# Kernel optimization log

Hardware: AMD Instinct MI355X
Metric: run time of the kernel (lower is better)

The kernel has to match this reference:

```python
import jax, jax.numpy as jnp
import numpy as np

N_NODES = 100000
N_EDGES = 1600000


def setup_inputs() -> dict:
    key = jax.random.key(0)
    k1, k2, k3, k4 = jax.random.split(key, 4)
    x = jax.random.normal(k1, (N_NODES, 16), dtype=jnp.float32)
    edge_index = jax.random.randint(k2, (2, N_EDGES), 0, N_NODES, dtype=jnp.int32)
    # Glorot-ish init for the two GCN layers
    W1 = jax.random.normal(k3, (16, 32), dtype=jnp.float32) * (1.0 / np.sqrt(16))
    b1 = jnp.zeros((32,), dtype=jnp.float32)
    W2 = jax.random.normal(k4, (32, 2), dtype=jnp.float32) * (1.0 / np.sqrt(32))
    b2 = jnp.zeros((2,), dtype=jnp.float32)
    return {"x": x, "edge_index": edge_index, "W1": W1, "b1": b1, "W2": W2, "b2": b2}


def _gcn_conv(x, W, b, src, dst, norm, n_nodes):
    # PyG GCNConv: h = X @ W; aggregate norm * h[src] at dst; add bias.
    h = x @ W                                   # [N, out]
    msg = h[src] * norm[:, None]                # [E+N, out] gather + scale
    out = jax.ops.segment_sum(msg, dst, num_segments=n_nodes)
    return out + b


def reference(x, edge_index, W1, b1, W2, b2):
    n = x.shape[0]
    self_loops = jnp.arange(n, dtype=edge_index.dtype)
    src = jnp.concatenate([edge_index[0], self_loops])  # [E+N]
    dst = jnp.concatenate([edge_index[1], self_loops])
    # Symmetric GCN normalization: deg computed on graph with self-loops
    deg = jax.ops.segment_sum(jnp.ones_like(dst, dtype=x.dtype), dst, num_segments=n)
    dis = jnp.where(deg > 0, jax.lax.rsqrt(deg), 0.0)   # deg^{-1/2}
    norm = dis[src] * dis[dst]                          # [E+N]

    h = jax.nn.relu(_gcn_conv(x, W1, b1, src, dst, norm, n))
    out = _gcn_conv(h, W2, b2, src, dst, norm, n)
    return out
```

## Files before the change

kernel.cpp:

```cpp
#include <hip/hip_runtime.h>
#include <hip/hip_fp16.h>

static constexpr int N  = 100000;
static constexpr int E  = 1600000;
static constexpr int B  = 256;
static constexpr int BG = 512;

static constexpr int BC     = 1024;
static constexpr int NBLKC  = 256;
static constexpr int CHUNKC = E / NBLKC;
static constexpr int CH2    = CHUNKC / 2;
static constexpr int PER2   = (CH2 + BC - 1) / BC;
static constexpr int NBUCK  = (N + 127) / 128;
static constexpr int SLAB   = 3072;
static constexpr int GCS    = 16;


__global__ __launch_bounds__(BC) void kC_scatter(
        const int2* __restrict__ src2, const int2* __restrict__ dst2,
        int* __restrict__ gcur, int* __restrict__ gslab) {
    __shared__ int lhist[NBUCK];
    __shared__ int gb[NBUCK];

    int t = threadIdx.x, blk = blockIdx.x;
    for (int i = t; i < NBUCK; i += BC) lhist[i] = 0;
    __syncthreads();

    int eb2 = blk * CH2;
    int2 dsv[PER2], ssv[PER2];
#pragma unroll
    for (int k = 0; k < PER2; ++k) {
        int idx = k * BC + t;
        if (idx < CH2) {
            dsv[k] = dst2[eb2 + idx];
            ssv[k] = src2[eb2 + idx];
            atomicAdd(&lhist[dsv[k].x >> 7], 1);
            atomicAdd(&lhist[dsv[k].y >> 7], 1);
        }
    }
    __syncthreads();

    if (t < NBUCK) {
        int h = lhist[t];
        if (h > 0) gb[t] = t * SLAB + atomicAdd(&gcur[t * GCS], h);
        lhist[t] = 0;
    }
    __syncthreads();

#pragma unroll
    for (int k = 0; k < PER2; ++k) {
        int idx = k * BC + t;
        if (idx < CH2) {
            {
                int d = dsv[k].x, b = d >> 7;
                int r = atomicAdd(&lhist[b], 1);
                int g = gb[b] + r;
                if (g < (b + 1) * SLAB)
                    gslab[g] = ssv[k].x | ((d & 127) << 17);
            }
            {
                int d = dsv[k].y, b = d >> 7;
                int r = atomicAdd(&lhist[b], 1);
                int g = gb[b] + r;
                if (g < (b + 1) * SLAB)
                    gslab[g] = ssv[k].y | ((d & 127) << 17);
            }
        }
    }
}


__global__ void kD1_deg(const int* __restrict__ gcur, const int* __restrict__ gslab,
                        int* __restrict__ rofs, const float4* __restrict__ x4,
                        __half* __restrict__ xpre) {
    __shared__ int c[128];
    __shared__ int wq[2];
    int t = threadIdx.x, b = blockIdx.x;
    if (t < 128) c[t] = 0;
    __syncthreads();

    int ne = min(gcur[b * GCS], SLAB);
    int base = b * SLAB;
    int ne4 = ne & ~3;
    for (int k = 4 * t; k < ne4; k += 4 * B) {
        int4 p4 = *(const int4*)(gslab + base + k);
        atomicAdd(&c[p4.x >> 17], 1);
        atomicAdd(&c[p4.y >> 17], 1);
        atomicAdd(&c[p4.z >> 17], 1);
        atomicAdd(&c[p4.w >> 17], 1);
    }
    if (t < ne - ne4) atomicAdd(&c[gslab[base + ne4 + t] >> 17], 1);
    __syncthreads();

    int lane = t & 63, wv = t >> 6;
    int val = (t < 128) ? c[t] : 0;
    int inc = val;
#pragma unroll
    for (int off = 1; off < 64; off <<= 1) {
        int u = __shfl_up(inc, off, 64);
        if (lane >= off) inc += u;
    }
    if (t == 63) wq[0] = inc;
    __syncthreads();
    if (t < 128) rofs[b * 129 + t] = base + inc - val + ((wv == 1) ? wq[0] : 0);
    if (t == 128) rofs[b * 129 + 128] = base + ne;

    int n = b * 128 + (t >> 1), h = t & 1;
    if (n < N) {
        float d = rsqrtf((float)(c[t >> 1] + 1));
        float4 u0 = x4[(size_t)n * 4 + h * 2];
        float4 u1 = x4[(size_t)n * 4 + h * 2 + 1];
        ushort4 p0, p1;
        p0.x = __half_as_ushort(__float2half(u0.x * d));
        p0.y = __half_as_ushort(__float2half(u0.y * d));
        p0.z = __half_as_ushort(__float2half(u0.z * d));
        p0.w = __half_as_ushort(__float2half(u0.w * d));
        p1.x = __half_as_ushort(__float2half(u1.x * d));
        p1.y = __half_as_ushort(__float2half(u1.y * d));
        p1.z = __half_as_ushort(__float2half(u1.z * d));
        p1.w = __half_as_ushort(__float2half(u1.w * d));
        *(ushort4*)(xpre + (size_t)n * 16 + h * 8)     = p0;
        *(ushort4*)(xpre + (size_t)n * 16 + h * 8 + 4) = p1;
    }
}


__global__ __launch_bounds__(BG) void kD2_agg(
        const __half* __restrict__ xpre, int* __restrict__ gslab,
        const int* __restrict__ rofs, const float* __restrict__ W1,
        const float* __restrict__ b1, const float* __restrict__ W2,
        float2* __restrict__ hpre) {
    __shared__ int st1[SLAB];
    __shared__ int cur[128];
    __shared__ int lofs[129];
    __shared__ float acc[128 * 17];
    __shared__ float sW1[512], sb1[32], sW2[64];
    int t = threadIdx.x, b = blockIdx.x;
    sW1[t] = W1[t];
    if (t < 32) sb1[t] = b1[t];
    if (t < 64) sW2[t] = W2[t];
    if (t < 128) cur[t] = 0;
    int base = b * SLAB;
    if (t < 129) lofs[t] = rofs[b * 129 + t] - base;
    __syncthreads();

    int ne = lofs[128];
    for (int k = t; k < ne; k += BG) {
        int p = gslab[base + k];
        int lo = p >> 17;
        int r = atomicAdd(&cur[lo], 1);
        st1[lofs[lo] + r] = p & 0x1FFFF;
    }
    __syncthreads();

    int ne4 = ne & ~3;
    for (int k = 4 * t; k < ne4; k += 4 * BG)
        *(int4*)(gslab + base + k) = *(const int4*)(st1 + k);
    for (int k = ne4 + t; k < ne; k += BG)
        gslab[base + k] = st1[k];

    int h = t & 1, e = (t >> 1) & 1, nl = t >> 2;
    int n = b * 128 + nl;
    float a0 = 0.f, a1 = 0.f, a2 = 0.f, a3 = 0.f,
          a4 = 0.f, a5 = 0.f, a6 = 0.f, a7 = 0.f;
    if (n < N) {
        auto add8 = [&](int4 w) {
            float2 q0 = __half22float2(*(__half2*)&w.x);
            float2 q1 = __half22float2(*(__half2*)&w.y);
            float2 q2 = __half22float2(*(__half2*)&w.z);
            float2 q3 = __half22float2(*(__half2*)&w.w);
            a0 += q0.x; a1 += q0.y; a2 += q1.x; a3 += q1.y;
            a4 += q2.x; a5 += q2.y; a6 += q3.x; a7 += q3.y;
        };
        int rs = lofs[nl], re = lofs[nl + 1];
        if (e == 0)
            add8(*(const int4*)(xpre + (size_t)n * 16 + h * 8));
        int k = rs + e;
        for (; k + 6 < re; k += 8) {
            int s0 = st1[k], s1 = st1[k + 2], s2 = st1[k + 4], s3 = st1[k + 6];
            int4 v0 = *(const int4*)(xpre + (size_t)s0 * 16 + h * 8);
            int4 v1 = *(const int4*)(xpre + (size_t)s1 * 16 + h * 8);
            int4 v2 = *(const int4*)(xpre + (size_t)s2 * 16 + h * 8);
            int4 v3 = *(const int4*)(xpre + (size_t)s3 * 16 + h * 8);
            add8(v0); add8(v1); add8(v2); add8(v3);
        }
        for (; k < re; k += 2)
            add8(*(const int4*)(xpre + (size_t)st1[k] * 16 + h * 8));
    }
    a0 += __shfl_xor(a0, 2, 64); a1 += __shfl_xor(a1, 2, 64);
    a2 += __shfl_xor(a2, 2, 64); a3 += __shfl_xor(a3, 2, 64);
    a4 += __shfl_xor(a4, 2, 64); a5 += __shfl_xor(a5, 2, 64);
    a6 += __shfl_xor(a6, 2, 64); a7 += __shfl_xor(a7, 2, 64);
    if (n < N && e == 0) {
        float* row = acc + nl * 17 + h * 8;
        row[0] = a0; row[1] = a1; row[2] = a2; row[3] = a3;
        row[4] = a4; row[5] = a5; row[6] = a6; row[7] = a7;
    }
    __syncthreads();

    if (t < 128) {
        int n2 = b * 128 + t;
        if (n2 < N) {
            int deg = lofs[t + 1] - lofs[t];
            float d = rsqrtf((float)(deg + 1));
            const float* row = acc + t * 17;
            float xi[16];
#pragma unroll
            for (int k = 0; k < 16; ++k) xi[k] = row[k] * d;
            float o0 = 0.f, o1 = 0.f;
#pragma unroll
            for (int c = 0; c < 32; ++c) {
                float hh = sb1[c];
#pragma unroll
                for (int k = 0; k < 16; ++k) hh = fmaf(xi[k], sW1[k * 32 + c], hh);
                hh = fmaxf(hh, 0.f);
                o0 = fmaf(hh, sW2[c * 2 + 0], o0);
                o1 = fmaf(hh, sW2[c * 2 + 1], o1);
            }
            hpre[n2] = make_float2(d * o0, d * o1);
        }
    }
}


__global__ __launch_bounds__(BG) void kF_l2(
        const float2* __restrict__ hpre, const int* __restrict__ gslab,
        const int* __restrict__ rofs, const float* __restrict__ b2,
        float2* __restrict__ out) {
    __shared__ int st1[SLAB];
    __shared__ int lofs[129];
    int t = threadIdx.x, b = blockIdx.x;
    int base = b * SLAB;
    if (t < 129) lofs[t] = rofs[b * 129 + t] - base;
    __syncthreads();

    int ne = lofs[128];
    int ne4 = ne & ~3;
    for (int k = 4 * t; k < ne4; k += 4 * BG)
        *(int4*)(st1 + k) = *(const int4*)(gslab + base + k);
    for (int k = ne4 + t; k < ne; k += BG)
        st1[k] = gslab[base + k];
    __syncthreads();

    int e = t & 3, nl = t >> 2;
    int n = b * 128 + nl;
    float o0 = 0.f, o1 = 0.f;
    int deg = 0;
    if (n < N) {
        int rs = lofs[nl], re = lofs[nl + 1];
        deg = re - rs;
        if (e == 0) {
            float2 self = hpre[n];
            o0 = self.x; o1 = self.y;
        }
        int k = rs + e;
        for (; k + 12 < re; k += 16) {
            float2 v0 = hpre[st1[k]];
            float2 v1 = hpre[st1[k + 4]];
            float2 v2 = hpre[st1[k + 8]];
            float2 v3 = hpre[st1[k + 12]];
            o0 += (v0.x + v1.x) + (v2.x + v3.x);
            o1 += (v0.y + v1.y) + (v2.y + v3.y);
        }
        for (; k < re; k += 4) {
            float2 v = hpre[st1[k]];
            o0 += v.x; o1 += v.y;
        }
    }
    o0 += __shfl_xor(o0, 1, 64); o1 += __shfl_xor(o1, 1, 64);
    o0 += __shfl_xor(o0, 2, 64); o1 += __shfl_xor(o1, 2, 64);
    if (n < N && e == 0) {
        float d = rsqrtf((float)(deg + 1));
        out[n] = make_float2(fmaf(d, o0, b2[0]), fmaf(d, o1, b2[1]));
    }
}


extern "C" void kernel_launch(void* const* d_in, const int* in_sizes, int n_in,
                              void* d_out, int out_size, void* d_ws, size_t ws_size,
                              hipStream_t stream) {
    const float* x  = (const float*)d_in[0];
    const int*   ei = (const int*)d_in[1];
    const float* W1 = (const float*)d_in[2];
    const float* b1 = (const float*)d_in[3];
    const float* W2 = (const float*)d_in[4];
    const float* b2 = (const float*)d_in[5];

    const int2* src2 = (const int2*)ei;
    const int2* dst2 = (const int2*)(ei + E);

    int*    gslab = (int*)d_ws;
    int*    rofs  = gslab + (size_t)NBUCK * SLAB;
    int*    gcur  = rofs + 100880;
    float*  hpre  = (float*)(gcur + 12512);
    __half* xpre  = (__half*)(hpre + 2 * (size_t)N);

    hipMemsetAsync(gcur, 0, NBUCK * GCS * sizeof(int), stream);
    kC_scatter<<<NBLKC, BC, 0, stream>>>(src2, dst2, gcur, gslab);
    kD1_deg<<<NBUCK, B, 0, stream>>>(gcur, gslab, rofs, (const float4*)x, xpre);
    kD2_agg<<<NBUCK, BG, 0, stream>>>(xpre, gslab, rofs, W1, b1, W2, (float2*)hpre);
    kF_l2<<<NBUCK, BG, 0, stream>>>((const float2*)hpre, gslab, rofs, b2,
                                    (float2*)d_out);
}
```

Baseline: 129.0 us.

## Count node degrees via global atomics in scatter, simplify degree kernel to scan

Moves per-node degree counting into the scatter kernel using global atomics on a new deg array, so the second kernel no longer re-reads the slab to build histograms. The second kernel becomes a per-node scan with one thread per node, writing row offsets and prescaled half-precision features. The scatter grid is also enlarged to 500 blocks. This trades a slab re-read for about 1.6M scattered global atomics, which may contend.

```diff
diff --git a/kernel.cpp b/kernel.cpp
--- a/kernel.cpp
+++ b/kernel.cpp
@@ -3,11 +3,11 @@
 
 static constexpr int N  = 100000;
 static constexpr int E  = 1600000;
-static constexpr int B  = 256;
+static constexpr int B1 = 128;
 static constexpr int BG = 512;
 
 static constexpr int BC     = 1024;
-static constexpr int NBLKC  = 256;
+static constexpr int NBLKC  = 500;
 static constexpr int CHUNKC = E / NBLKC;
 static constexpr int CH2    = CHUNKC / 2;
 static constexpr int PER2   = (CH2 + BC - 1) / BC;
@@ -18,7 +18,8 @@
 
 __global__ __launch_bounds__(BC) void kC_scatter(
         const int2* __restrict__ src2, const int2* __restrict__ dst2,
-        int* __restrict__ gcur, int* __restrict__ gslab) {
+        int* __restrict__ gcur, int* __restrict__ gslab,
+        int* __restrict__ deg) {
     __shared__ int lhist[NBUCK];
     __shared__ int gb[NBUCK];
 
@@ -36,6 +37,8 @@
             ssv[k] = src2[eb2 + idx];
             atomicAdd(&lhist[dsv[k].x >> 7], 1);
             atomicAdd(&lhist[dsv[k].y >> 7], 1);
+            atomicAdd(&deg[dsv[k].x], 1);
+            atomicAdd(&deg[dsv[k].y], 1);
         }
     }
     __syncthreads();
@@ -70,47 +73,35 @@
 }
 
 
-__global__ void kD1_deg(const int* __restrict__ gcur, const int* __restrict__ gslab,
-                        int* __restrict__ rofs, const float4* __restrict__ x4,
-                        __half* __restrict__ xpre) {
-    __shared__ int c[128];
-    __shared__ int wq[2];
+__global__ __launch_bounds__(B1) void kD1_scan(
+        const int* __restrict__ deg, int* __restrict__ rofs,
+        const float4* __restrict__ x4, __half* __restrict__ xpre) {
+    __shared__ int wq;
     int t = threadIdx.x, b = blockIdx.x;
-    if (t < 128) c[t] = 0;
-    __syncthreads();
-
-    int ne = min(gcur[b * GCS], SLAB);
-    int base = b * SLAB;
-    int ne4 = ne & ~3;
-    for (int k = 4 * t; k < ne4; k += 4 * B) {
-        int4 p4 = *(const int4*)(gslab + base + k);
-        atomicAdd(&c[p4.x >> 17], 1);
-        atomicAdd(&c[p4.y >> 17], 1);
-        atomicAdd(&c[p4.z >> 17], 1);
-        atomicAdd(&c[p4.w >> 17], 1);
-    }
-    if (t < ne - ne4) atomicAdd(&c[gslab[base + ne4 + t] >> 17], 1);
-    __syncthreads();
-
-    int lane = t & 63, wv = t >> 6;
-    int val = (t < 128) ? c[t] : 0;
-    int inc = val;
+    int n = b * 128 + t;
+    int dg = (n < N) ? deg[n] : 0;
+
+    int wv = t >> 6;
+    int inc = dg;
 #pragma unroll
     for (int off = 1; off < 64; off <<= 1) {
         int u = __shfl_up(inc, off, 64);
-        if (lane >= off) inc += u;
-    }
-    if (t == 63) wq[0] = inc;
-    __syncthreads();
-    if (t < 128) rofs[b * 129 + t] = base + inc - val + ((wv == 1) ? wq[0] : 0);
-    if (t == 128) rofs[b * 129 + 128] = base + ne;
-
-    int n = b * 128 + (t >> 1), h = t & 1;
+        if ((t & 63) >= off) inc += u;
+    }
+    if (t == 63) wq = inc;
+    __syncthreads();
+    int ex = inc - dg + ((wv == 1) ? wq : 0);
+    int base = b * SLAB;
+    rofs[b * 129 + t] = base + ex;
+    if (t == 127) rofs[b * 129 + 128] = base + ex + dg;
+
     if (n < N) {
-        float d = rsqrtf((float)(c[t >> 1] + 1));
-        float4 u0 = x4[(size_t)n * 4 + h * 2];
-        float4 u1 = x4[(size_t)n * 4 + h * 2 + 1];
-        ushort4 p0, p1;
+        float d = rsqrtf((float)(dg + 1));
+        float4 u0 = x4[(size_t)n * 4 + 0];
+        float4 u1 = x4[(size_t)n * 4 + 1];
+        float4 u2 = x4[(size_t)n * 4 + 2];
+        float4 u3 = x4[(size_t)n * 4 + 3];
+        ushort4 p0, p1, p2, p3;
         p0.x = __half_as_ushort(__float2half(u0.x * d));
         p0.y = __half_as_ushort(__float2half(u0.y * d));
         p0.z = __half_as_ushort(__float2half(u0.z * d));
@@ -119,8 +110,18 @@
         p1.y = __half_as_ushort(__float2half(u1.y * d));
         p1.z = __half_as_ushort(__float2half(u1.z * d));
         p1.w = __half_as_ushort(__float2half(u1.w * d));
-        *(ushort4*)(xpre + (size_t)n * 16 + h * 8)     = p0;
-        *(ushort4*)(xpre + (size_t)n * 16 + h * 8 + 4) = p1;
+        p2.x = __half_as_ushort(__float2half(u2.x * d));
+        p2.y = __half_as_ushort(__float2half(u2.y * d));
+        p2.z = __half_as_ushort(__float2half(u2.z * d));
+        p2.w = __half_as_ushort(__float2half(u2.w * d));
+        p3.x = __half_as_ushort(__float2half(u3.x * d));
+        p3.y = __half_as_ushort(__float2half(u3.y * d));
+        p3.z = __half_as_ushort(__float2half(u3.z * d));
+        p3.w = __half_as_ushort(__float2half(u3.w * d));
+        *(ushort4*)(xpre + (size_t)n * 16)      = p0;
+        *(ushort4*)(xpre + (size_t)n * 16 + 4)  = p1;
+        *(ushort4*)(xpre + (size_t)n * 16 + 8)  = p2;
+        *(ushort4*)(xpre + (size_t)n * 16 + 12) = p3;
     }
 }
 
@@ -292,12 +293,13 @@
     int*    gslab = (int*)d_ws;
     int*    rofs  = gslab + (size_t)NBUCK * SLAB;
     int*    gcur  = rofs + 100880;
-    float*  hpre  = (float*)(gcur + 12512);
+    int*    deg   = gcur + 12512;
+    float*  hpre  = (float*)(deg + 100000);
     __half* xpre  = (__half*)(hpre + 2 * (size_t)N);
 
-    hipMemsetAsync(gcur, 0, NBUCK * GCS * sizeof(int), stream);
-    kC_scatter<<<NBLKC, BC, 0, stream>>>(src2, dst2, gcur, gslab);
-    kD1_deg<<<NBUCK, B, 0, stream>>>(gcur, gslab, rofs, (const float4*)x, xpre);
+    hipMemsetAsync(gcur, 0, (NBUCK * GCS + N) * sizeof(int), stream);
+    kC_scatter<<<NBLKC, BC, 0, stream>>>(src2, dst2, gcur, gslab, deg);
+    kD1_scan<<<NBUCK, B1, 0, stream>>>(deg, rofs, (const float4*)x, xpre);
     kD2_agg<<<NBUCK, BG, 0, stream>>>(xpre, gslab, rofs, W1, b1, W2, (float2*)hpre);
     kF_l2<<<NBUCK, BG, 0, stream>>>((const float2*)hpre, gslab, rofs, b2,
                                     (float2*)d_out);
```

Result: slower. 191.7 us (+48.6%).
